# Kernel tuning notes

Measured on AMD Instinct MI355X. Metric: run time of the kernel, lower is better.

Reference implementation:

```python
import jax, jax.numpy as jnp
import numpy as np

B, IN_F, OUT_F = 1024, 512, 512


def setup_inputs() -> dict:
    key = jax.random.key(0)
    k1, k2 = jax.random.split(key)
    x = jax.random.uniform(k1, (B, IN_F), dtype=jnp.float32)
    weight = jax.random.uniform(k2, (IN_F, OUT_F), dtype=jnp.float32)
    return {"x": x, "weight": weight}


def reference(x, weight):
    # Max-min fuzzy composition (tropical semiring 'matmul'):
    # out[b, o] = max_i min(x[b, i], W[i, o])
    # x: [B, IN], weight: [IN, OUT] -> out: [B, OUT]
    return jnp.max(jnp.minimum(x[:, :, None], weight[None, :, :]), axis=1)
```

## Files before the change

kernel.cpp:

```cpp
#include <hip/hip_runtime.h>


typedef __fp16 h2 __attribute__((ext_vector_type(2)));
typedef __fp16 h4 __attribute__((ext_vector_type(4)));
typedef float f4 __attribute__((ext_vector_type(4)));
typedef unsigned int u32;
typedef u32 u32x4 __attribute__((ext_vector_type(4)));

#define IN_F 512
#define OUT_F 512
#define XS_BYTES (64 * 128)
#define WS_BYTES (64 * 128)
#define BUF_BYTES (XS_BYTES + WS_BYTES)

union U32H2 { u32 u; h2 h; };
static __device__ __forceinline__ h2 as_h2(u32 v) { U32H2 c; c.u = v; return c.h; }
static __device__ __forceinline__ u32 as_u32(h2 v) { U32H2 c; c.h = v; return c.u; }

static __device__ __forceinline__ h2 cvt2(float a, float b) {
  return __builtin_bit_cast(h2, __builtin_amdgcn_cvt_pkrtz(a, b));
}

__global__ __launch_bounds__(512) void maxmin_fused(const float* __restrict__ X,
                                                    const float* __restrict__ W,
                                                    float* __restrict__ Out) {
  __shared__ __align__(16) char smem[2 * BUF_BYTES];

  const int tid  = threadIdx.x;
  const int wv   = tid >> 6;
  const int lane = tid & 63;
  const int ty   = lane >> 3;
  const int tx   = lane & 7;
  const int b0   = blockIdx.x * 32;
  const int o0   = blockIdx.y * 64;

  const int xrow = tid & 31;
  const int xc4  = tid >> 5;
  const float* xg = X + (b0 + xrow) * IN_F + xc4 * 4;

  const int wrow = tid >> 4;
  const int wc4  = tid & 15;
  const float* wg = W + wrow * OUT_F + o0 + wc4 * 4;

  const int xs_r = (wv * 8) * 128 + ty * 16;
  const int ws_r = XS_BYTES + (wv * 8) * 128 + tx * 16;

  const int xw = xrow * 4;
  const int ww = XS_BYTES + wrow * 128 + wc4 * 8;

  h2 acc[4][4] = {};

  auto stage = [&](char* buf, f4 xv, f4 wva, f4 wvb) {
    *(h2*)(buf + (4 * xc4 + 0) * 128 + xw) = cvt2(xv.x, xv.x);
    *(h2*)(buf + (4 * xc4 + 1) * 128 + xw) = cvt2(xv.y, xv.y);
    *(h2*)(buf + (4 * xc4 + 2) * 128 + xw) = cvt2(xv.z, xv.z);
    *(h2*)(buf + (4 * xc4 + 3) * 128 + xw) = cvt2(xv.w, xv.w);
    h2 a0 = cvt2(wva.x, wva.y), a1 = cvt2(wva.z, wva.w);
    h4 pa = {a0.x, a0.y, a1.x, a1.y};
    *(h4*)(buf + ww) = pa;
    h2 b0h = cvt2(wvb.x, wvb.y), b1h = cvt2(wvb.z, wvb.w);
    h4 pb = {b0h.x, b0h.y, b1h.x, b1h.y};
    *(h4*)(buf + 32 * 128 + ww) = pb;
  };

  f4 xf = *(const f4*)xg;
  f4 wa = *(const f4*)wg;
  f4 wb = *(const f4*)(wg + 32 * OUT_F);
  stage(smem, xf, wa, wb);
  __syncthreads();

  for (int c = 0; c < 8; ++c) {
    f4 nx, na, nb;
    if (c < 7) {
      nx = *(const f4*)(xg + (c + 1) * 64);
      na = *(const f4*)(wg + (c + 1) * 64 * OUT_F);
      nb = *(const f4*)(wg + (c + 1) * 64 * OUT_F + 32 * OUT_F);
    }
    const char* bufc = smem + (c & 1) * BUF_BYTES;
#pragma unroll
    for (int j = 0; j < 8; ++j) {
      u32x4 xq = *(const u32x4*)(bufc + xs_r + j * 128);
      u32x4 wq = *(const u32x4*)(bufc + ws_r + j * 128);
#pragma unroll
      for (int i = 0; i < 4; ++i) {
        const h2 xv = as_h2(xq[i]);
#pragma unroll
        for (int jj = 0; jj < 4; ++jj) {
          const h2 mn = __builtin_elementwise_min(xv, as_h2(wq[jj]));
          acc[i][jj] = __builtin_elementwise_max(acc[i][jj], mn);
        }
      }
    }
    if (c < 7) stage(smem + ((c + 1) & 1) * BUF_BYTES, nx, na, nb);
    __syncthreads();
  }

#pragma unroll
  for (int i = 0; i < 4; ++i) {
    u32x4 v = {as_u32(acc[i][0]), as_u32(acc[i][1]), as_u32(acc[i][2]), as_u32(acc[i][3])};
    *(u32x4*)(smem + wv * 4096 + (4 * ty + i) * 128 + tx * 16) = v;
  }
  __syncthreads();

  const int orow = tid >> 4;
  const int oco  = (tid & 15) * 4;
  const int cb   = orow * 128 + oco * 2;
  h4 m = *(const h4*)(smem + cb);
#pragma unroll
  for (int g = 1; g < 8; ++g) {
    h4 v = *(const h4*)(smem + g * 4096 + cb);
    m = __builtin_elementwise_max(m, v);
  }
  f4 o = {(float)m.x, (float)m.y, (float)m.z, (float)m.w};
  *(f4*)(Out + (b0 + orow) * OUT_F + o0 + oco) = o;
}

extern "C" void kernel_launch(void* const* d_in, const int* in_sizes, int n_in,
                              void* d_out, int out_size, void* d_ws, size_t ws_size,
                              hipStream_t stream) {
  const float* x = (const float*)d_in[0];
  const float* w = (const float*)d_in[1];
  float* out = (float*)d_out;
  (void)in_sizes; (void)n_in; (void)out_size; (void)d_ws; (void)ws_size;
  dim3 grid(1024 / 32, 512 / 64);
  maxmin_fused<<<grid, 512, 0, stream>>>(x, w, out);
}
```

Baseline: 72.98 us.

## Use 1024-thread blocks with 16-way K split and unsigned-int packed min/max

Doubles the block to 16 waves, each covering a quarter of a 64-wide K chunk, which halves the per-thread inner loop and the per-thread staging loads. It then reduces 16 partial results through shared memory instead of 8. The fp16 packed min/max is replaced by unsigned 16-bit min/max, which gives the same ordering for the non-negative inputs used here. The intent is more waves in flight, at the cost of a larger cross-wave reduction and a 64KB shared-memory allocation, which may limit occupancy.

Result: faster. 68.87 us (-5.6%).

```diff
diff --git a/kernel.cpp b/kernel.cpp
--- a/kernel.cpp
+++ b/kernel.cpp
@@ -1,30 +1,39 @@
 #include <hip/hip_runtime.h>
 
 
+typedef unsigned int u32;
+typedef unsigned short u16;
+typedef u16 u16x2 __attribute__((ext_vector_type(2)));
+typedef u32 u32x2 __attribute__((ext_vector_type(2)));
+typedef u32 u32x4 __attribute__((ext_vector_type(4)));
+typedef float f4 __attribute__((ext_vector_type(4)));
+typedef float f2 __attribute__((ext_vector_type(2)));
 typedef __fp16 h2 __attribute__((ext_vector_type(2)));
-typedef __fp16 h4 __attribute__((ext_vector_type(4)));
-typedef float f4 __attribute__((ext_vector_type(4)));
-typedef unsigned int u32;
-typedef u32 u32x4 __attribute__((ext_vector_type(4)));
 
 #define IN_F 512
 #define OUT_F 512
-#define XS_BYTES (64 * 128)
-#define WS_BYTES (64 * 128)
+#define XS_BYTES 8192
+#define WS_BYTES 8192
 #define BUF_BYTES (XS_BYTES + WS_BYTES)
 
-union U32H2 { u32 u; h2 h; };
-static __device__ __forceinline__ h2 as_h2(u32 v) { U32H2 c; c.u = v; return c.h; }
-static __device__ __forceinline__ u32 as_u32(h2 v) { U32H2 c; c.h = v; return c.u; }
-
-static __device__ __forceinline__ h2 cvt2(float a, float b) {
-  return __builtin_bit_cast(h2, __builtin_amdgcn_cvt_pkrtz(a, b));
+static __device__ __forceinline__ u32 pkcvt(float a, float b) {
+  return __builtin_bit_cast(u32, __builtin_amdgcn_cvt_pkrtz(a, b));
+}
+static __device__ __forceinline__ u32 pkmin(u32 a, u32 b) {
+  u16x2 r = __builtin_elementwise_min(__builtin_bit_cast(u16x2, a),
+                                      __builtin_bit_cast(u16x2, b));
+  return __builtin_bit_cast(u32, r);
+}
+static __device__ __forceinline__ u32 pkmax(u32 a, u32 b) {
+  u16x2 r = __builtin_elementwise_max(__builtin_bit_cast(u16x2, a),
+                                      __builtin_bit_cast(u16x2, b));
+  return __builtin_bit_cast(u32, r);
 }
 
-__global__ __launch_bounds__(512) void maxmin_fused(const float* __restrict__ X,
-                                                    const float* __restrict__ W,
-                                                    float* __restrict__ Out) {
-  __shared__ __align__(16) char smem[2 * BUF_BYTES];
+__global__ __launch_bounds__(1024, 4) void maxmin_v2(const float* __restrict__ X,
+                                                     const float* __restrict__ W,
+                                                     float* __restrict__ Out) {
+  __shared__ __align__(16) char smem[65536];
 
   const int tid  = threadIdx.x;
   const int wv   = tid >> 6;
@@ -35,84 +44,76 @@
   const int o0   = blockIdx.y * 64;
 
   const int xrow = tid & 31;
-  const int xc4  = tid >> 5;
-  const float* xg = X + (b0 + xrow) * IN_F + xc4 * 4;
+  const int xq   = tid >> 5;
+  const bool dox = (xq < 16);
+  const float* xg = X + (b0 + xrow) * IN_F + xq * 4;
 
   const int wrow = tid >> 4;
   const int wc4  = tid & 15;
   const float* wg = W + wrow * OUT_F + o0 + wc4 * 4;
 
-  const int xs_r = (wv * 8) * 128 + ty * 16;
-  const int ws_r = XS_BYTES + (wv * 8) * 128 + tx * 16;
+  const int xs_r = (wv * 4) * 128 + ty * 16;
+  const int ws_r = XS_BYTES + (wv * 4) * 128 + tx * 16;
 
   const int xw = xrow * 4;
   const int ww = XS_BYTES + wrow * 128 + wc4 * 8;
 
-  h2 acc[4][4] = {};
+  u32 acc[4][4] = {};
 
-  auto stage = [&](char* buf, f4 xv, f4 wva, f4 wvb) {
-    *(h2*)(buf + (4 * xc4 + 0) * 128 + xw) = cvt2(xv.x, xv.x);
-    *(h2*)(buf + (4 * xc4 + 1) * 128 + xw) = cvt2(xv.y, xv.y);
-    *(h2*)(buf + (4 * xc4 + 2) * 128 + xw) = cvt2(xv.z, xv.z);
-    *(h2*)(buf + (4 * xc4 + 3) * 128 + xw) = cvt2(xv.w, xv.w);
-    h2 a0 = cvt2(wva.x, wva.y), a1 = cvt2(wva.z, wva.w);
-    h4 pa = {a0.x, a0.y, a1.x, a1.y};
-    *(h4*)(buf + ww) = pa;
-    h2 b0h = cvt2(wvb.x, wvb.y), b1h = cvt2(wvb.z, wvb.w);
-    h4 pb = {b0h.x, b0h.y, b1h.x, b1h.y};
-    *(h4*)(buf + 32 * 128 + ww) = pb;
+  auto stage = [&](char* buf, f4 xv, f4 wv4) {
+    u32x2 wp = {pkcvt(wv4.x, wv4.y), pkcvt(wv4.z, wv4.w)};
+    *(u32x2*)(buf + ww) = wp;
+    if (dox) {
+      *(u32*)(buf + (4 * xq + 0) * 128 + xw) = pkcvt(xv.x, xv.x);
+      *(u32*)(buf + (4 * xq + 1) * 128 + xw) = pkcvt(xv.y, xv.y);
+      *(u32*)(buf + (4 * xq + 2) * 128 + xw) = pkcvt(xv.z, xv.z);
+      *(u32*)(buf + (4 * xq + 3) * 128 + xw) = pkcvt(xv.w, xv.w);
+    }
   };
 
-  f4 xf = *(const f4*)xg;
-  f4 wa = *(const f4*)wg;
-  f4 wb = *(const f4*)(wg + 32 * OUT_F);
-  stage(smem, xf, wa, wb);
+  f4 xv = {};
+  if (dox) xv = *(const f4*)xg;
+  f4 wv4 = *(const f4*)wg;
+  stage(smem, xv, wv4);
   __syncthreads();
 
   for (int c = 0; c < 8; ++c) {
-    f4 nx, na, nb;
+    f4 nx = {}, nw = {};
     if (c < 7) {
-      nx = *(const f4*)(xg + (c + 1) * 64);
-      na = *(const f4*)(wg + (c + 1) * 64 * OUT_F);
-      nb = *(const f4*)(wg + (c + 1) * 64 * OUT_F + 32 * OUT_F);
+      if (dox) nx = *(const f4*)(xg + (c + 1) * 64);
+      nw = *(const f4*)(wg + (c + 1) * 64 * OUT_F);
     }
-    const char* bufc = smem + (c & 1) * BUF_BYTES;
+    const char* buf = smem + (c & 1) * BUF_BYTES;
 #pragma unroll
-    for (int j = 0; j < 8; ++j) {
-      u32x4 xq = *(const u32x4*)(bufc + xs_r + j * 128);
-      u32x4 wq = *(const u32x4*)(bufc + ws_r + j * 128);
+    for (int j = 0; j < 4; ++j) {
+      u32x4 xqv = *(const u32x4*)(buf + xs_r + j * 128);
+      u32x4 wqv = *(const u32x4*)(buf + ws_r + j * 128);
 #pragma unroll
-      for (int i = 0; i < 4; ++i) {
-        const h2 xv = as_h2(xq[i]);
+      for (int i = 0; i < 4; ++i)
 #pragma unroll
-        for (int jj = 0; jj < 4; ++jj) {
-          const h2 mn = __builtin_elementwise_min(xv, as_h2(wq[jj]));
-          acc[i][jj] = __builtin_elementwise_max(acc[i][jj], mn);
-        }
-      }
+        for (int jj = 0; jj < 4; ++jj)
+          acc[i][jj] = pkmax(acc[i][jj], pkmin(xqv[i], wqv[jj]));
     }
-    if (c < 7) stage(smem + ((c + 1) & 1) * BUF_BYTES, nx, na, nb);
+    if (c < 7) stage(smem + ((c + 1) & 1) * BUF_BYTES, nx, nw);
     __syncthreads();
   }
 
 #pragma unroll
   for (int i = 0; i < 4; ++i) {
-    u32x4 v = {as_u32(acc[i][0]), as_u32(acc[i][1]), as_u32(acc[i][2]), as_u32(acc[i][3])};
+    u32x4 v = {acc[i][0], acc[i][1], acc[i][2], acc[i][3]};
     *(u32x4*)(smem + wv * 4096 + (4 * ty + i) * 128 + tx * 16) = v;
   }
   __syncthreads();
 
-  const int orow = tid >> 4;
-  const int oco  = (tid & 15) * 4;
-  const int cb   = orow * 128 + oco * 2;
-  h4 m = *(const h4*)(smem + cb);
+  const int row = tid >> 5;
+  const int cp  = tid & 31;
+  const int cb  = row * 128 + cp * 4;
+  u32 m = *(const u32*)(smem + cb);
 #pragma unroll
-  for (int g = 1; g < 8; ++g) {
-    h4 v = *(const h4*)(smem + g * 4096 + cb);
-    m = __builtin_elementwise_max(m, v);
-  }
-  f4 o = {(float)m.x, (float)m.y, (float)m.z, (float)m.w};
-  *(f4*)(Out + (b0 + orow) * OUT_F + o0 + oco) = o;
+  for (int g = 1; g < 16; ++g) m = pkmax(m, *(const u32*)(smem + g * 4096 + cb));
+  h2 hm = __builtin_bit_cast(h2, m);
+  f2 o = {(float)hm.x, (float)hm.y};
+  *(f2*)(Out + (b0 + row) * OUT_F + o0 + cp * 2) = o;
 }
 
 extern "C" void kernel_launch(void* const* d_in, const int* in_sizes, int n_in,
@@ -123,5 +124,5 @@
   float* out = (float*)d_out;
   (void)in_sizes; (void)n_in; (void)out_size; (void)d_ws; (void)ws_size;
   dim3 grid(1024 / 32, 512 / 64);
-  maxmin_fused<<<grid, 512, 0, stream>>>(x, w, out);
+  maxmin_v2<<<grid, 1024, 0, stream>>>(x, w, out);
 }
```
